# Kernel tuning notes

Hardware: AMD Instinct MI355X
Metric: run time of the kernel (lower is better)

Reference implementation:

```python
import jax, jax.numpy as jnp
import numpy as np

B, M, FIN, FOUT, K, E = 4, 50000, 128, 128, 4, 800000


def setup_inputs() -> dict:
    key = jax.random.key(0)
    ks = jax.random.split(key, 8)
    x = jax.random.normal(ks[0], (B, M, FIN), dtype=jnp.float32)
    L_rows = jax.random.randint(ks[1], (E,), 0, M, dtype=jnp.int32)
    L_cols = jax.random.randint(ks[2], (E,), 0, M, dtype=jnp.int32)
    # stands in for the rescaled (0.75 * (2L/lmax - I)) Laplacian values
    L_vals = jax.random.normal(ks[3], (E,), dtype=jnp.float32) * 0.05
    stddev = 1.0 / np.sqrt(FIN * (K + 0.5) / 2.0)
    kernel = jax.random.normal(ks[4], (K * FIN, FOUT), dtype=jnp.float32) * stddev
    W_down = jax.random.normal(ks[5], (FOUT, FOUT // 8), dtype=jnp.float32) * (1.0 / np.sqrt(FOUT))
    b_down = jnp.zeros((FOUT // 8,), dtype=jnp.float32)
    W_up = jax.random.normal(ks[6], (FOUT // 8, FOUT), dtype=jnp.float32) * (1.0 / np.sqrt(FOUT // 8))
    b_up = jnp.zeros((FOUT,), dtype=jnp.float32)
    return {"x": x, "L_vals": L_vals, "L_rows": L_rows, "L_cols": L_cols,
            "kernel": kernel, "W_down": W_down, "b_down": b_down,
            "W_up": W_up, "b_up": b_up}


def reference(x, L_vals, L_rows, L_cols, kernel, W_down, b_down, W_up, b_up):
    B_, M_, Fin = x.shape
    K_ = kernel.shape[0] // Fin

    def spmm(X):  # sparse L [M,M] @ dense X [M, D]
        return jax.ops.segment_sum(L_vals[:, None] * X[L_cols], L_rows, num_segments=M_)

    # Chebyshev recurrence, operating on [M, Fin*B] like the TF code
    x0 = x.transpose(1, 2, 0).reshape(M_, Fin * B_)
    stack = [x0]
    if K_ > 1:
        x1 = spmm(x0)
        stack.append(x1)
    for _ in range(2, K_):
        x2 = 2.0 * spmm(x1) - x0
        stack.append(x2)
        x0, x1 = x1, x2

    # [K,M,Fin*B] -> [K,M,Fin,B] -> [B,M,Fin,K] -> [B*M, Fin*K]
    xs = jnp.stack(stack, axis=0).reshape(K_, M_, Fin, B_)
    xs = xs.transpose(3, 1, 2, 0).reshape(B_ * M_, Fin * K_)
    y = (xs @ kernel).reshape(B_, M_, -1)
    y = jax.nn.relu(y)

    # SE block: avg-pool over nodes, down (swish), up (sigmoid), scale
    s = jnp.mean(y, axis=1, keepdims=True)          # [B, 1, Fout]
    d = jax.nn.swish(s @ W_down + b_down)           # [B, 1, Fout/8]
    u = jax.nn.sigmoid(d @ W_up + b_up)             # [B, 1, Fout]
    return y * u
```

## Files before the change

### kernel.cpp

```cpp
#include <hip/hip_runtime.h>
#include <hip/hip_bf16.h>

#define BB 4
#define MM 50000
#define FINF 128
#define FOUTF 128
#define KCH 4
#define EE 800000
#define NROWS (BB*MM)
#define XC 512
#define CD 512

__device__ __forceinline__ float bf2f(unsigned short u){
    union{unsigned int i; float f;} v; v.i = ((unsigned int)u) << 16; return v.f;
}
__device__ __forceinline__ unsigned short f2bf(float f){
    union{float f; unsigned int i;} v; v.f = f;
    unsigned int r = v.i + 0x7FFF + ((v.i >> 16) & 1);
    return (unsigned short)(r >> 16);
}

typedef __bf16 bf16x8 __attribute__((ext_vector_type(8)));
typedef float  f32x4  __attribute__((ext_vector_type(4)));

__global__ __launch_bounds__(256) void k_init_x0(const float* __restrict__ x,
                                                 unsigned short* __restrict__ X0){
    int tid = blockIdx.x*256 + threadIdx.x;
    if (tid >= BB*MM*FINF/4) return;
    int f4 = tid & 31;
    int t  = tid >> 5;
    int m  = t % MM, b = t / MM;
    float4 v = ((const float4*)x)[tid];
    ushort4 o;
    o.x = f2bf(v.x); o.y = f2bf(v.y); o.z = f2bf(v.z); o.w = f2bf(v.w);
    *(ushort4*)(X0 + (size_t)m*XC + b*FINF + f4*4) = o;
}

__global__ __launch_bounds__(256) void k_prepw(const float* __restrict__ kern,
                                               unsigned short* __restrict__ Wt){
    int tid = blockIdx.x*256 + threadIdx.x;
    int c = tid & 511, n = tid >> 9;
    int kc = c >> 7, f = c & 127;
    int ns = n >> 4, l16 = n & 15;
    int ks = c >> 5, rem = c & 31, g = rem >> 3, j = rem & 7;
    int lane = g*16 + l16;
    Wt[((ns*16 + ks)*64 + lane)*8 + j] = f2bf(kern[(f*KCH + kc)*FOUTF + n]);
}

__global__ __launch_bounds__(256) void k_hist(const int* __restrict__ rows, int* __restrict__ counts){
    int e = blockIdx.x*256 + threadIdx.x;
    if (e < EE) atomicAdd(&counts[rows[e]], 1);
}

__global__ __launch_bounds__(1024) void k_scan(const int* __restrict__ counts,
                                               int* __restrict__ offs, int* __restrict__ cursor){
    __shared__ int part[1024];
    const int CH = (MM + 1023) / 1024;
    int t = threadIdx.x;
    int lo = t*CH; if (lo > MM) lo = MM;
    int hi = lo + CH; if (hi > MM) hi = MM;
    int s = 0;
    for (int i = lo; i < hi; ++i) s += counts[i];
    part[t] = s; __syncthreads();
    for (int d = 1; d < 1024; d <<= 1){
        int v = (t >= d) ? part[t-d] : 0;
        __syncthreads();
        part[t] += v;
        __syncthreads();
    }
    int run = (t == 0) ? 0 : part[t-1];
    for (int i = lo; i < hi; ++i){
        offs[i] = run; cursor[i] = run; run += counts[i];
    }
    if (t == 1023) offs[MM] = part[1023];
}

__global__ __launch_bounds__(256) void k_scatter(const int* __restrict__ rows, const int* __restrict__ cols,
                                                 const float* __restrict__ vals, int* __restrict__ cursor,
                                                 int* __restrict__ colv, float* __restrict__ valv){
    int e = blockIdx.x*256 + threadIdx.x;
    if (e >= EE) return;
    int r = rows[e];
    int pos = atomicAdd(&cursor[r], 1);
    colv[pos] = cols[e]; valv[pos] = vals[e];
}

__global__ __launch_bounds__(128) void k_spmm(const unsigned short* __restrict__ Xin,
                                              const unsigned short* __restrict__ Xprev,
                                              unsigned short* __restrict__ Xout,
                                              const int* __restrict__ offs,
                                              const int* __restrict__ colv,
                                              const float* __restrict__ valv,
                                              float alpha, int sub){
    int m = blockIdx.x, t = threadIdx.x;
    int c0 = t*4;
    int start = offs[m], end = offs[m+1];
    float a0=0.f, a1=0.f, a2=0.f, a3=0.f;
    for (int j = start; j < end; ++j){
        int col = colv[j]; float val = valv[j];
        ushort4 xv = *(const ushort4*)(Xin + (size_t)col*XC + c0);
        a0 += val*bf2f(xv.x); a1 += val*bf2f(xv.y);
        a2 += val*bf2f(xv.z); a3 += val*bf2f(xv.w);
    }
    a0 *= alpha; a1 *= alpha; a2 *= alpha; a3 *= alpha;
    if (sub){
        ushort4 pv = *(const ushort4*)(Xprev + (size_t)m*XC + c0);
        a0 -= bf2f(pv.x); a1 -= bf2f(pv.y); a2 -= bf2f(pv.z); a3 -= bf2f(pv.w);
    }
    ushort4 o; o.x = f2bf(a0); o.y = f2bf(a1); o.z = f2bf(a2); o.w = f2bf(a3);
    *(ushort4*)(Xout + (size_t)m*XC + c0) = o;
}

__global__ __launch_bounds__(256, 2) void k_gemm(const unsigned short* __restrict__ X0,
                                                 const unsigned short* __restrict__ X1,
                                                 const unsigned short* __restrict__ X2,
                                                 const unsigned short* __restrict__ X3,
                                                 const unsigned short* __restrict__ Wt,
                                                 float* __restrict__ Y){
    const int wave = threadIdx.x >> 6;
    const int lane = threadIdx.x & 63;
    const int l16  = lane & 15;
    const int g    = lane >> 4;
    const int r0   = blockIdx.x*256 + wave*64;

    int aoff[4];
    #pragma unroll
    for (int i = 0; i < 4; ++i){
        int ra = r0 + i*16 + l16;
        if (ra >= NROWS) ra = NROWS-1;
        aoff[i] = (ra % MM)*XC + (ra / MM)*FINF + g*8;
    }

    const unsigned short* const Xs[4] = {X0, X1, X2, X3};

    f32x4 acc[4][8];
    #pragma unroll
    for (int i = 0; i < 4; ++i)
        #pragma unroll
        for (int j = 0; j < 8; ++j) acc[i][j] = (f32x4){0.f,0.f,0.f,0.f};

    bf16x8 a_cur[4], b_cur[8], a_nxt[4], b_nxt[8];

    {
        const unsigned short* Xb = Xs[0];
        #pragma unroll
        for (int i = 0; i < 4; ++i) a_cur[i] = *(const bf16x8*)(Xb + aoff[i]);
        #pragma unroll
        for (int ns = 0; ns < 8; ++ns) b_cur[ns] = *(const bf16x8*)(Wt + (ns*16)*512 + lane*8);
    }

    #pragma unroll
    for (int ks = 0; ks < 16; ++ks){
        if (ks < 15){
            const int kn = ks + 1;
            const unsigned short* Xb = Xs[kn >> 2];
            const int f0 = (kn & 3)*32;
            #pragma unroll
            for (int i = 0; i < 4; ++i) a_nxt[i] = *(const bf16x8*)(Xb + aoff[i] + f0);
            #pragma unroll
            for (int ns = 0; ns < 8; ++ns) b_nxt[ns] = *(const bf16x8*)(Wt + (ns*16 + kn)*512 + lane*8);
        }
        #pragma unroll
        for (int ns = 0; ns < 8; ++ns)
            #pragma unroll
            for (int i = 0; i < 4; ++i)
                acc[i][ns] = __builtin_amdgcn_mfma_f32_16x16x32_bf16(a_cur[i], b_cur[ns], acc[i][ns], 0, 0, 0);
        #pragma unroll
        for (int i = 0; i < 4; ++i) a_cur[i] = a_nxt[i];
        #pragma unroll
        for (int ns = 0; ns < 8; ++ns) b_cur[ns] = b_nxt[ns];
    }

    #pragma unroll
    for (int i = 0; i < 4; ++i){
        #pragma unroll
        for (int reg = 0; reg < 4; ++reg){
            int r = r0 + i*16 + g*4 + reg;
            if (r < NROWS){
                #pragma unroll
                for (int ns = 0; ns < 8; ++ns){
                    float v = acc[i][ns][reg];
                    Y[(size_t)r*FOUTF + ns*16 + l16] = v > 0.f ? v : 0.f;
                }
            }
        }
    }
}

__global__ __launch_bounds__(256) void k_colmean(const float* __restrict__ Y, float* __restrict__ sacc){
    int b = blockIdx.y, t = threadIdx.x;
    int c4 = t & 31, rs = t >> 5;
    const int rows = (MM + gridDim.x - 1) / gridDim.x;
    int m0 = blockIdx.x * rows;
    int mend = m0 + rows; if (mend > MM) mend = MM;
    float4 s = {0.f,0.f,0.f,0.f};
    for (int m = m0 + rs; m < mend; m += 8){
        float4 v = *(const float4*)(Y + ((size_t)b*MM + m)*FOUTF + c4*4);
        s.x += v.x; s.y += v.y; s.z += v.z; s.w += v.w;
    }
    __shared__ float4 red[8][32];
    red[rs][c4] = s;
    __syncthreads();
    if (t < 32){
        float4 a = red[0][t];
        #pragma unroll
        for (int i = 1; i < 8; ++i){
            float4 v = red[i][t];
            a.x += v.x; a.y += v.y; a.z += v.z; a.w += v.w;
        }
        atomicAdd(&sacc[b*FOUTF + t*4 + 0], a.x);
        atomicAdd(&sacc[b*FOUTF + t*4 + 1], a.y);
        atomicAdd(&sacc[b*FOUTF + t*4 + 2], a.z);
        atomicAdd(&sacc[b*FOUTF + t*4 + 3], a.w);
    }
}

__global__ __launch_bounds__(128) void k_se(const float* __restrict__ sacc,
                                            const float* __restrict__ Wd, const float* __restrict__ bd,
                                            const float* __restrict__ Wu, const float* __restrict__ bu,
                                            float* __restrict__ u){
    int b = blockIdx.x, t = threadIdx.x;
    __shared__ float sm[128];
    __shared__ float dsh[16];
    sm[t] = sacc[b*FOUTF + t] * (1.0f/MM);
    __syncthreads();
    if (t < 16){
        float a = bd[t];
        for (int f = 0; f < 128; ++f) a += sm[f]*Wd[f*16 + t];
        dsh[t] = a / (1.f + expf(-a));
    }
    __syncthreads();
    float a = bu[t];
    for (int j = 0; j < 16; ++j) a += dsh[j]*Wu[j*FOUTF + t];
    u[b*FOUTF + t] = 1.f/(1.f + expf(-a));
}

__global__ __launch_bounds__(256) void k_scale(const float* __restrict__ Y, const float* __restrict__ u,
                                               float* __restrict__ out){
    int tid = blockIdx.x*256 + threadIdx.x;
    if (tid >= NROWS*FOUTF/4) return;
    int b  = tid / (MM*FOUTF/4);
    int f4 = tid & 31;
    float4 yv = ((const float4*)Y)[tid];
    float4 uv = *(const float4*)(u + b*FOUTF + f4*4);
    float4 o;
    o.x = yv.x*uv.x; o.y = yv.y*uv.y; o.z = yv.z*uv.z; o.w = yv.w*uv.w;
    ((float4*)out)[tid] = o;
}

extern "C" void kernel_launch(void* const* d_in, const int* in_sizes, int n_in,
                              void* d_out, int out_size, void* d_ws, size_t ws_size,
                              hipStream_t stream){
    (void)in_sizes; (void)n_in; (void)out_size; (void)ws_size;
    const float* x    = (const float*)d_in[0];
    const float* lv   = (const float*)d_in[1];
    const int*   lr   = (const int*)d_in[2];
    const int*   lc   = (const int*)d_in[3];
    const float* kern = (const float*)d_in[4];
    const float* Wd   = (const float*)d_in[5];
    const float* bd   = (const float*)d_in[6];
    const float* Wu   = (const float*)d_in[7];
    const float* bu   = (const float*)d_in[8];
    float* out = (float*)d_out;

    char* w = (char*)d_ws;
    size_t off = 0;
    auto take = [&](size_t bytes)->char*{
        char* p = w + off; off += (bytes + 255) & ~(size_t)255; return p;
    };
    unsigned short* X[4];
    for (int i = 0; i < 4; ++i) X[i] = (unsigned short*)take((size_t)MM*XC*2);
    float* Y           = (float*)take((size_t)NROWS*FOUTF*4);
    unsigned short* Wt = (unsigned short*)take((size_t)FOUTF*CD*2);
    int* counts        = (int*)take((size_t)MM*4);
    int* offs          = (int*)take((size_t)(MM+1)*4);
    int* cursor        = (int*)take((size_t)MM*4);
    int* colv          = (int*)take((size_t)EE*4);
    float* valv        = (float*)take((size_t)EE*4);
    float* sacc        = (float*)take((size_t)BB*FOUTF*4);
    float* u           = (float*)take((size_t)BB*FOUTF*4);

    hipMemsetAsync(counts, 0, MM*4, stream);
    hipMemsetAsync(sacc, 0, BB*FOUTF*4, stream);

    k_init_x0<<<25000, 256, 0, stream>>>(x, X[0]);
    k_prepw<<<256, 256, 0, stream>>>(kern, Wt);
    k_hist<<<(EE+255)/256, 256, 0, stream>>>(lr, counts);
    k_scan<<<1, 1024, 0, stream>>>(counts, offs, cursor);
    k_scatter<<<(EE+255)/256, 256, 0, stream>>>(lr, lc, lv, cursor, colv, valv);

    k_spmm<<<MM, 128, 0, stream>>>(X[0], X[0], X[1], offs, colv, valv, 1.0f, 0);
    k_spmm<<<MM, 128, 0, stream>>>(X[1], X[0], X[2], offs, colv, valv, 2.0f, 1);
    k_spmm<<<MM, 128, 0, stream>>>(X[2], X[1], X[3], offs, colv, valv, 2.0f, 1);

    k_gemm<<<(NROWS+255)/256, 256, 0, stream>>>(X[0], X[1], X[2], X[3], Wt, Y);

    dim3 gmean(256, BB);
    k_colmean<<<gmean, 256, 0, stream>>>(Y, sacc);
    k_se<<<BB, 128, 0, stream>>>(sacc, Wd, bd, Wu, bu, u);
    k_scale<<<25000, 256, 0, stream>>>(Y, u, out);
}
```

Baseline: 914.8 us.

## Slice feature layout into 64-byte column slices for XCD-local SpMM gathers

Stores the Chebyshev feature matrices as 16 column slices of 32 bf16 each (one contiguous [M,32] array per slice) instead of interleaved 512-wide rows. The SpMM grid is reorganised so each block handles 32 rows of one slice, and slices are mapped to XCDs via the block index so each XCD's L2 holds a smaller working set for the random column gathers. Edge column and value are packed into one int2 array to halve index loads. The GEMM addressing is updated for the new layout; the risk is that each edge list is now re-read once per slice, 16 times per row instead of once.

```diff
diff --git a/kernel.cpp b/kernel.cpp
--- a/kernel.cpp
+++ b/kernel.cpp
@@ -10,6 +10,7 @@
 #define NROWS (BB*MM)
 #define XC 512
 #define CD 512
+#define SLICE_ELEMS (MM*32)
 
 __device__ __forceinline__ float bf2f(unsigned short u){
     union{unsigned int i; float f;} v; v.i = ((unsigned int)u) << 16; return v.f;
@@ -22,6 +23,7 @@
 
 typedef __bf16 bf16x8 __attribute__((ext_vector_type(8)));
 typedef float  f32x4  __attribute__((ext_vector_type(4)));
+
 
 __global__ __launch_bounds__(256) void k_init_x0(const float* __restrict__ x,
                                                  unsigned short* __restrict__ X0){
@@ -33,7 +35,9 @@
     float4 v = ((const float4*)x)[tid];
     ushort4 o;
     o.x = f2bf(v.x); o.y = f2bf(v.y); o.z = f2bf(v.z); o.w = f2bf(v.w);
-    *(ushort4*)(X0 + (size_t)m*XC + b*FINF + f4*4) = o;
+    int s = b*4 + (f4 >> 3);
+    int inner = (f4 & 7)*4;
+    *(ushort4*)(X0 + (size_t)s*SLICE_ELEMS + m*32 + inner) = o;
 }
 
 __global__ __launch_bounds__(256) void k_prepw(const float* __restrict__ kern,
@@ -77,38 +81,58 @@
 
 __global__ __launch_bounds__(256) void k_scatter(const int* __restrict__ rows, const int* __restrict__ cols,
                                                  const float* __restrict__ vals, int* __restrict__ cursor,
-                                                 int* __restrict__ colv, float* __restrict__ valv){
+                                                 int2* __restrict__ edges){
     int e = blockIdx.x*256 + threadIdx.x;
     if (e >= EE) return;
     int r = rows[e];
     int pos = atomicAdd(&cursor[r], 1);
-    colv[pos] = cols[e]; valv[pos] = vals[e];
-}
-
-__global__ __launch_bounds__(128) void k_spmm(const unsigned short* __restrict__ Xin,
+    int2 ev; ev.x = cols[e]; ev.y = __float_as_int(vals[e]);
+    edges[pos] = ev;
+}
+
+__global__ __launch_bounds__(256) void k_spmm(const unsigned short* __restrict__ Xin,
                                               const unsigned short* __restrict__ Xprev,
                                               unsigned short* __restrict__ Xout,
                                               const int* __restrict__ offs,
-                                              const int* __restrict__ colv,
-                                              const float* __restrict__ valv,
+                                              const int2* __restrict__ edges,
                                               float alpha, int sub){
-    int m = blockIdx.x, t = threadIdx.x;
-    int c0 = t*4;
-    int start = offs[m], end = offs[m+1];
+    const int NRB = (MM + 31) / 32;
+    const int G2  = NRB * 8;
+    int b = blockIdx.x;
+    int phase = b / G2;
+    int w     = b % G2;
+    int xcd   = w & 7;
+    int rowblock = w >> 3;
+    int slice = xcd*2 + phase;
+
+    int lane = threadIdx.x & 63;
+    int wv   = threadIdx.x >> 6;
+    int c    = lane & 7;
+    int rsub = lane >> 3;
+    int r = rowblock*32 + wv*8 + rsub;
+    bool valid = r < MM;
+    int rc = valid ? r : MM-1;
+
+    const unsigned short* Xs = Xin + slice*SLICE_ELEMS;
+    int start = offs[rc], end = offs[rc+1];
     float a0=0.f, a1=0.f, a2=0.f, a3=0.f;
     for (int j = start; j < end; ++j){
-        int col = colv[j]; float val = valv[j];
-        ushort4 xv = *(const ushort4*)(Xin + (size_t)col*XC + c0);
+        int2 e = edges[j];
+        float val = __int_as_float(e.y);
+        ushort4 xv = *(const ushort4*)(Xs + e.x*32 + c*4);
         a0 += val*bf2f(xv.x); a1 += val*bf2f(xv.y);
         a2 += val*bf2f(xv.z); a3 += val*bf2f(xv.w);
     }
-    a0 *= alpha; a1 *= alpha; a2 *= alpha; a3 *= alpha;
-    if (sub){
-        ushort4 pv = *(const ushort4*)(Xprev + (size_t)m*XC + c0);
-        a0 -= bf2f(pv.x); a1 -= bf2f(pv.y); a2 -= bf2f(pv.z); a3 -= bf2f(pv.w);
-    }
-    ushort4 o; o.x = f2bf(a0); o.y = f2bf(a1); o.z = f2bf(a2); o.w = f2bf(a3);
-    *(ushort4*)(Xout + (size_t)m*XC + c0) = o;
+    if (valid){
+        a0 *= alpha; a1 *= alpha; a2 *= alpha; a3 *= alpha;
+        int o = slice*SLICE_ELEMS + r*32 + c*4;
+        if (sub){
+            ushort4 pv = *(const ushort4*)(Xprev + o);
+            a0 -= bf2f(pv.x); a1 -= bf2f(pv.y); a2 -= bf2f(pv.z); a3 -= bf2f(pv.w);
+        }
+        ushort4 ov; ov.x = f2bf(a0); ov.y = f2bf(a1); ov.z = f2bf(a2); ov.w = f2bf(a3);
+        *(ushort4*)(Xout + o) = ov;
+    }
 }
 
 __global__ __launch_bounds__(256, 2) void k_gemm(const unsigned short* __restrict__ X0,
@@ -128,7 +152,7 @@
     for (int i = 0; i < 4; ++i){
         int ra = r0 + i*16 + l16;
         if (ra >= NROWS) ra = NROWS-1;
-        aoff[i] = (ra % MM)*XC + (ra / MM)*FINF + g*8;
+        aoff[i] = (ra / MM)*(4*SLICE_ELEMS) + (ra % MM)*32 + g*8;
     }
 
     const unsigned short* const Xs[4] = {X0, X1, X2, X3};
@@ -154,7 +178,7 @@
         if (ks < 15){
             const int kn = ks + 1;
             const unsigned short* Xb = Xs[kn >> 2];
-            const int f0 = (kn & 3)*32;
+            const int f0 = (kn & 3)*SLICE_ELEMS;
             #pragma unroll
             for (int i = 0; i < 4; ++i) a_nxt[i] = *(const bf16x8*)(Xb + aoff[i] + f0);
             #pragma unroll
@@ -275,8 +299,7 @@
     int* counts        = (int*)take((size_t)MM*4);
     int* offs          = (int*)take((size_t)(MM+1)*4);
     int* cursor        = (int*)take((size_t)MM*4);
-    int* colv          = (int*)take((size_t)EE*4);
-    float* valv        = (float*)take((size_t)EE*4);
+    int2* edges        = (int2*)take((size_t)EE*8);
     float* sacc        = (float*)take((size_t)BB*FOUTF*4);
     float* u           = (float*)take((size_t)BB*FOUTF*4);
 
@@ -287,11 +310,13 @@
     k_prepw<<<256, 256, 0, stream>>>(kern, Wt);
     k_hist<<<(EE+255)/256, 256, 0, stream>>>(lr, counts);
     k_scan<<<1, 1024, 0, stream>>>(counts, offs, cursor);
-    k_scatter<<<(EE+255)/256, 256, 0, stream>>>(lr, lc, lv, cursor, colv, valv);
-
-    k_spmm<<<MM, 128, 0, stream>>>(X[0], X[0], X[1], offs, colv, valv, 1.0f, 0);
-    k_spmm<<<MM, 128, 0, stream>>>(X[1], X[0], X[2], offs, colv, valv, 2.0f, 1);
-    k_spmm<<<MM, 128, 0, stream>>>(X[2], X[1], X[3], offs, colv, valv, 2.0f, 1);
+    k_scatter<<<(EE+255)/256, 256, 0, stream>>>(lr, lc, lv, cursor, edges);
+
+    const int NRB = (MM + 31) / 32;
+    const int SPMM_GRID = NRB * 16;
+    k_spmm<<<SPMM_GRID, 256, 0, stream>>>(X[0], X[0], X[1], offs, edges, 1.0f, 0);
+    k_spmm<<<SPMM_GRID, 256, 0, stream>>>(X[1], X[0], X[2], offs, edges, 2.0f, 1);
+    k_spmm<<<SPMM_GRID, 256, 0, stream>>>(X[2], X[1], X[3], offs, edges, 2.0f, 1);
 
     k_gemm<<<(NROWS+255)/256, 256, 0, stream>>>(X[0], X[1], X[2], X[3], Wt, Y);
 
```

After: 1.114 ms. 21.8% more time.

## Restructure SpMM to one wave per row with packed edges and 16-byte loads

Applied to the files above, without the earlier changes.

Packs column index and value into a single int2 edge array, and rewrites the SpMM kernel so each 64-lane wave handles one row. Each lane now loads 8 bf16 values (16 bytes) instead of 4, and the edge loop is unrolled by four so more independent gathers are in flight. This aims to cut per-block overhead, raise memory-level parallelism for the random row gathers, and reduce index-load traffic. It adds register pressure, and a row with few edges leaves most of the unrolled loop unused.

```diff
diff --git a/kernel.cpp b/kernel.cpp
--- a/kernel.cpp
+++ b/kernel.cpp
@@ -22,6 +22,7 @@
 
 typedef __bf16 bf16x8 __attribute__((ext_vector_type(8)));
 typedef float  f32x4  __attribute__((ext_vector_type(4)));
+typedef unsigned short u16x8 __attribute__((ext_vector_type(8)));
 
 __global__ __launch_bounds__(256) void k_init_x0(const float* __restrict__ x,
                                                  unsigned short* __restrict__ X0){
@@ -77,38 +78,69 @@
 
 __global__ __launch_bounds__(256) void k_scatter(const int* __restrict__ rows, const int* __restrict__ cols,
                                                  const float* __restrict__ vals, int* __restrict__ cursor,
-                                                 int* __restrict__ colv, float* __restrict__ valv){
+                                                 int2* __restrict__ edges){
     int e = blockIdx.x*256 + threadIdx.x;
     if (e >= EE) return;
     int r = rows[e];
     int pos = atomicAdd(&cursor[r], 1);
-    colv[pos] = cols[e]; valv[pos] = vals[e];
-}
-
-__global__ __launch_bounds__(128) void k_spmm(const unsigned short* __restrict__ Xin,
+    int2 ev; ev.x = cols[e]; ev.y = __float_as_int(vals[e]);
+    edges[pos] = ev;
+}
+
+__global__ __launch_bounds__(256) void k_spmm(const unsigned short* __restrict__ Xin,
                                               const unsigned short* __restrict__ Xprev,
                                               unsigned short* __restrict__ Xout,
                                               const int* __restrict__ offs,
-                                              const int* __restrict__ colv,
-                                              const float* __restrict__ valv,
+                                              const int2* __restrict__ edges,
                                               float alpha, int sub){
-    int m = blockIdx.x, t = threadIdx.x;
-    int c0 = t*4;
-    int start = offs[m], end = offs[m+1];
-    float a0=0.f, a1=0.f, a2=0.f, a3=0.f;
-    for (int j = start; j < end; ++j){
-        int col = colv[j]; float val = valv[j];
-        ushort4 xv = *(const ushort4*)(Xin + (size_t)col*XC + c0);
-        a0 += val*bf2f(xv.x); a1 += val*bf2f(xv.y);
-        a2 += val*bf2f(xv.z); a3 += val*bf2f(xv.w);
-    }
-    a0 *= alpha; a1 *= alpha; a2 *= alpha; a3 *= alpha;
+    int wv   = threadIdx.x >> 6;
+    int lane = threadIdx.x & 63;
+    int r = __builtin_amdgcn_readfirstlane(blockIdx.x*4 + wv);
+    if (r >= MM) return;
+    int c0 = lane*8;
+    int start = offs[r], end = offs[r+1];
+
+    float acc[8];
+    #pragma unroll
+    for (int i = 0; i < 8; ++i) acc[i] = 0.f;
+
+    int j = start;
+    for (; j + 4 <= end; j += 4){
+        int2 e0 = edges[j], e1 = edges[j+1], e2 = edges[j+2], e3 = edges[j+3];
+        u16x8 x0 = *(const u16x8*)(Xin + (size_t)e0.x*XC + c0);
+        u16x8 x1 = *(const u16x8*)(Xin + (size_t)e1.x*XC + c0);
+        u16x8 x2 = *(const u16x8*)(Xin + (size_t)e2.x*XC + c0);
+        u16x8 x3 = *(const u16x8*)(Xin + (size_t)e3.x*XC + c0);
+        float v0 = __int_as_float(e0.y), v1 = __int_as_float(e1.y);
+        float v2 = __int_as_float(e2.y), v3 = __int_as_float(e3.y);
+        #pragma unroll
+        for (int i = 0; i < 8; ++i){
+            acc[i] += v0*bf2f(x0[i]);
+            acc[i] += v1*bf2f(x1[i]);
+            acc[i] += v2*bf2f(x2[i]);
+            acc[i] += v3*bf2f(x3[i]);
+        }
+    }
+    for (; j < end; ++j){
+        int2 e = edges[j];
+        u16x8 xv = *(const u16x8*)(Xin + (size_t)e.x*XC + c0);
+        float v = __int_as_float(e.y);
+        #pragma unroll
+        for (int i = 0; i < 8; ++i) acc[i] += v*bf2f(xv[i]);
+    }
+
+    size_t o = (size_t)r*XC + c0;
+    #pragma unroll
+    for (int i = 0; i < 8; ++i) acc[i] *= alpha;
     if (sub){
-        ushort4 pv = *(const ushort4*)(Xprev + (size_t)m*XC + c0);
-        a0 -= bf2f(pv.x); a1 -= bf2f(pv.y); a2 -= bf2f(pv.z); a3 -= bf2f(pv.w);
-    }
-    ushort4 o; o.x = f2bf(a0); o.y = f2bf(a1); o.z = f2bf(a2); o.w = f2bf(a3);
-    *(ushort4*)(Xout + (size_t)m*XC + c0) = o;
+        u16x8 pv = *(const u16x8*)(Xprev + o);
+        #pragma unroll
+        for (int i = 0; i < 8; ++i) acc[i] -= bf2f(pv[i]);
+    }
+    u16x8 ov;
+    #pragma unroll
+    for (int i = 0; i < 8; ++i) ov[i] = f2bf(acc[i]);
+    *(u16x8*)(Xout + o) = ov;
 }
 
 __global__ __launch_bounds__(256, 2) void k_gemm(const unsigned short* __restrict__ X0,
@@ -275,8 +307,7 @@
     int* counts        = (int*)take((size_t)MM*4);
     int* offs          = (int*)take((size_t)(MM+1)*4);
     int* cursor        = (int*)take((size_t)MM*4);
-    int* colv          = (int*)take((size_t)EE*4);
-    float* valv        = (float*)take((size_t)EE*4);
+    int2* edges        = (int2*)take((size_t)EE*8);
     float* sacc        = (float*)take((size_t)BB*FOUTF*4);
     float* u           = (float*)take((size_t)BB*FOUTF*4);
 
@@ -287,11 +318,11 @@
     k_prepw<<<256, 256, 0, stream>>>(kern, Wt);
     k_hist<<<(EE+255)/256, 256, 0, stream>>>(lr, counts);
     k_scan<<<1, 1024, 0, stream>>>(counts, offs, cursor);
-    k_scatter<<<(EE+255)/256, 256, 0, stream>>>(lr, lc, lv, cursor, colv, valv);
-
-    k_spmm<<<MM, 128, 0, stream>>>(X[0], X[0], X[1], offs, colv, valv, 1.0f, 0);
-    k_spmm<<<MM, 128, 0, stream>>>(X[1], X[0], X[2], offs, colv, valv, 2.0f, 1);
-    k_spmm<<<MM, 128, 0, stream>>>(X[2], X[1], X[3], offs, colv, valv, 2.0f, 1);
+    k_scatter<<<(EE+255)/256, 256, 0, stream>>>(lr, lc, lv, cursor, edges);
+
+    k_spmm<<<(MM+3)/4, 256, 0, stream>>>(X[0], X[0], X[1], offs, edges, 1.0f, 0);
+    k_spmm<<<(MM+3)/4, 256, 0, stream>>>(X[1], X[0], X[2], offs, edges, 2.0f, 1);
+    k_spmm<<<(MM+3)/4, 256, 0, stream>>>(X[2], X[1], X[3], offs, edges, 2.0f, 1);
 
     k_gemm<<<(NROWS+255)/256, 256, 0, stream>>>(X[0], X[1], X[2], X[3], Wt, Y);
 
```

Result: no change. 918.4 us (+0.4%).
